# Optimization experiments

Measured on AMD Instinct MI355X. Metric: run time of the kernel, lower is better.

The kernel has to match this reference:

```python
import jax, jax.numpy as jnp
import numpy as np

LN_EPS = 1e-12


def setup_inputs() -> dict:
    key = jax.random.key(0)
    ks = jax.random.split(key, 6)
    B, S, H = 32, 512, 768
    P, K = 76, 64
    V, E = 50257, 768
    return {
        "sequence_data": jax.random.normal(ks[0], (B, S, H), dtype=jnp.float32),
        "masked_positions": jax.random.randint(ks[1], (B, P), 0, S, dtype=jnp.int64),
        "candidate_sets": jax.random.randint(ks[2], (B, P, K), 0, V, dtype=jnp.int64),
        "embedding_table": jax.random.normal(ks[3], (V, E), dtype=jnp.float32) * 0.02,
        "dense_w": jax.random.normal(ks[4], (H, E), dtype=jnp.float32) * (1.0 / np.sqrt(H)),
        "dense_b": jnp.zeros((E,), dtype=jnp.float32),
        "ln_gamma": jnp.ones((E,), dtype=jnp.float32),
        "ln_beta": jnp.zeros((E,), dtype=jnp.float32),
    }


def reference(sequence_data, masked_positions, candidate_sets, embedding_table,
              dense_w, dense_b, ln_gamma, ln_beta):
    # Gather masked positions: [B, P, H]
    gathered = jnp.take_along_axis(
        sequence_data, masked_positions[:, :, None], axis=1)
    # Dense (no activation), then LayerNorm (eps=1e-12)
    lm = jnp.einsum('bph,he->bpe', gathered, dense_w) + dense_b
    mu = jnp.mean(lm, axis=-1, keepdims=True)
    var = jnp.mean(jnp.square(lm - mu), axis=-1, keepdims=True)
    lm = (lm - mu) * jax.lax.rsqrt(var + LN_EPS) * ln_gamma + ln_beta
    # Candidate embedding gather: [B, P, K, E]
    cand = embedding_table[candidate_sets]
    # Inner products -> logits [B, P, K]
    logits = jnp.einsum('bpe,bpke->bpk', lm, cand)
    return logits
```

## Files before the change

kernel.cpp:

```cpp
#include <hip/hip_runtime.h>

typedef __attribute__((ext_vector_type(8))) short bf16x8;
typedef __attribute__((ext_vector_type(4))) float f32x4;

#define HH 768
#define EE 768
#define BB 32
#define SS 512
#define PP 76
#define KCAND 64
#define MM (BB * PP)
#define VV 50257
#define NC (MM * KCAND)
#define CAP 16
#define OVF_CAP 4096

#define OFF_WT    0u
#define OFF_AG    1179648u
#define OFF_LM    4915200u
#define OFF_LMN   12386304u
#define OFF_CUR   16121856u
#define OFF_PERM2 16322896u
#define OFF_OVF   19539344u

#define WT_BLOCKS 576
#define AG_BLOCKS 304
#define ZR_BLOCKS 197
#define GEMM_BLOCKS 456
#define SC_BLOCKS 608
#define ROW_BLOCKS 12565
#define OVF_BLOCKS 32

__device__ inline unsigned short f2bf(float f) {
    unsigned int u = __float_as_uint(f);
    u += 0x7fffu + ((u >> 16) & 1u);
    return (unsigned short)(u >> 16);
}
__device__ inline float bf2f(unsigned short h) {
    return __uint_as_float(((unsigned int)h) << 16);
}

__global__ __launch_bounds__(256) void prep_kernel(
    const float* __restrict__ W, unsigned short* __restrict__ Wt,
    const float* __restrict__ seq, const int* __restrict__ mpos,
    unsigned short* __restrict__ Ag, int* __restrict__ cursor) {
    const int bid = blockIdx.x;
    if (bid < WT_BLOCKS) {
        __shared__ float tile[32][33];
        const int h0 = (bid % 24) * 32, e0 = (bid / 24) * 32;
        const int c = threadIdx.x & 31, r = threadIdx.x >> 5;
#pragma unroll
        for (int rr = r; rr < 32; rr += 8)
            tile[rr][c] = W[(size_t)(h0 + rr) * EE + e0 + c];
        __syncthreads();
#pragma unroll
        for (int rr = r; rr < 32; rr += 8)
            Wt[(size_t)(e0 + rr) * HH + h0 + c] = f2bf(tile[c][rr]);
    } else if (bid < WT_BLOCKS + AG_BLOCKS) {
        const int m0 = (bid - WT_BLOCKS) * 8;
        const int t = threadIdx.x;
#pragma unroll
        for (int rr = 0; rr < 8; ++rr) {
            const int m = m0 + rr;
            const int b = m / PP, p = m - b * PP;
            const int ps = mpos[b * PP + p];
            const float* srow = seq + (size_t)(b * SS + ps) * HH;
            unsigned short* drow = Ag + (size_t)m * HH;
#pragma unroll
            for (int j = 0; j < 3; ++j)
                drow[t + j * 256] = f2bf(srow[t + j * 256]);
        }
    } else {
        const int i = (bid - WT_BLOCKS - AG_BLOCKS) * 256 + threadIdx.x;
        if (i <= VV) cursor[i] = 0;
    }
}

__global__ __launch_bounds__(256) void gemm_scatter_kernel(
    const unsigned short* __restrict__ Ag, const unsigned short* __restrict__ Wt,
    float* __restrict__ lm, const int* __restrict__ cand,
    int* __restrict__ cursor, int* __restrict__ perm2, int* __restrict__ ovf) {
    const int bid = blockIdx.x;
    if (bid < GEMM_BLOCKS) {
        __shared__ unsigned short Alds[64][72];
        __shared__ unsigned short Blds[64][72];
        const int bn = bid % 12, bm = bid / 12;
        const int tid = threadIdx.x;
        const int sr = tid >> 2, sc = (tid & 3) * 16;
        const unsigned short* abase = Ag + (size_t)(bm * 64) * HH;
        const unsigned short* bbase = Wt + (size_t)(bn * 64) * HH;
        const int lane = tid & 63, wv = tid >> 6;
        const int wm = wv >> 1, wn = wv & 1;
        const int fr = lane & 15, fq = (lane >> 4) * 8;
        f32x4 acc[2][2] = {};
        for (int kk = 0; kk < HH; kk += 64) {
            __syncthreads();
            *(int4*)&Alds[sr][sc]     = *(const int4*)(abase + (size_t)sr * HH + kk + sc);
            *(int4*)&Alds[sr][sc + 8] = *(const int4*)(abase + (size_t)sr * HH + kk + sc + 8);
            *(int4*)&Blds[sr][sc]     = *(const int4*)(bbase + (size_t)sr * HH + kk + sc);
            *(int4*)&Blds[sr][sc + 8] = *(const int4*)(bbase + (size_t)sr * HH + kk + sc + 8);
            __syncthreads();
#pragma unroll
            for (int ks = 0; ks < 64; ks += 32) {
                bf16x8 af[2], bfr[2];
#pragma unroll
                for (int t = 0; t < 2; ++t)
                    af[t] = *(const bf16x8*)&Alds[wm * 32 + t * 16 + fr][ks + fq];
#pragma unroll
                for (int t = 0; t < 2; ++t)
                    bfr[t] = *(const bf16x8*)&Blds[wn * 32 + t * 16 + fr][ks + fq];
#pragma unroll
                for (int tm = 0; tm < 2; ++tm)
#pragma unroll
                    for (int tn = 0; tn < 2; ++tn)
                        acc[tm][tn] = __builtin_amdgcn_mfma_f32_16x16x32_bf16(
                            af[tm], bfr[tn], acc[tm][tn], 0, 0, 0);
            }
        }
#pragma unroll
        for (int tm = 0; tm < 2; ++tm)
#pragma unroll
            for (int tn = 0; tn < 2; ++tn) {
                const int col = bn * 64 + wn * 32 + tn * 16 + (lane & 15);
                const int rbase = bm * 64 + wm * 32 + tm * 16 + (lane >> 4) * 4;
#pragma unroll
                for (int g = 0; g < 4; ++g)
                    lm[(size_t)(rbase + g) * EE + col] = acc[tm][tn][g];
            }
    } else {
        const int i = (bid - GEMM_BLOCKS) * 256 + threadIdx.x;
        const int row = cand[i];
        const int slot = atomicAdd(&cursor[row], 1);
        if (slot < CAP) {
            perm2[row * CAP + slot] = i;
        } else {
            const int j = atomicAdd(&cursor[VV], 1);
            if (j < OVF_CAP) ovf[j] = i;
        }
    }
}

__global__ __launch_bounds__(256) void ln_kernel(
    const float* __restrict__ lm, const float* __restrict__ bias,
    const float* __restrict__ gamma, const float* __restrict__ beta,
    unsigned short* __restrict__ lmn) {
    const int lane = threadIdx.x & 63;
    const int m = blockIdx.x * 4 + (threadIdx.x >> 6);
    const float4* x4 = (const float4*)(lm + (size_t)m * EE);
    const float4* b4 = (const float4*)bias;
    const float4* g4 = (const float4*)gamma;
    const float4* e4 = (const float4*)beta;
    float x[12], g[12], e[12];
    {
        const float4 X0 = x4[lane * 2], X1 = x4[lane * 2 + 1], X2 = x4[128 + lane];
        const float4 B0 = b4[lane * 2], B1 = b4[lane * 2 + 1], B2 = b4[128 + lane];
        const float4 G0 = g4[lane * 2], G1 = g4[lane * 2 + 1], G2 = g4[128 + lane];
        const float4 E0 = e4[lane * 2], E1 = e4[lane * 2 + 1], E2 = e4[128 + lane];
        x[0]=X0.x+B0.x; x[1]=X0.y+B0.y; x[2]=X0.z+B0.z; x[3]=X0.w+B0.w;
        x[4]=X1.x+B1.x; x[5]=X1.y+B1.y; x[6]=X1.z+B1.z; x[7]=X1.w+B1.w;
        x[8]=X2.x+B2.x; x[9]=X2.y+B2.y; x[10]=X2.z+B2.z; x[11]=X2.w+B2.w;
        g[0]=G0.x; g[1]=G0.y; g[2]=G0.z; g[3]=G0.w;
        g[4]=G1.x; g[5]=G1.y; g[6]=G1.z; g[7]=G1.w;
        g[8]=G2.x; g[9]=G2.y; g[10]=G2.z; g[11]=G2.w;
        e[0]=E0.x; e[1]=E0.y; e[2]=E0.z; e[3]=E0.w;
        e[4]=E1.x; e[5]=E1.y; e[6]=E1.z; e[7]=E1.w;
        e[8]=E2.x; e[9]=E2.y; e[10]=E2.z; e[11]=E2.w;
    }
    float s = 0.f, q = 0.f;
#pragma unroll
    for (int i = 0; i < 12; ++i) { s += x[i]; q += x[i] * x[i]; }
#pragma unroll
    for (int m2 = 32; m2; m2 >>= 1) { s += __shfl_xor(s, m2); q += __shfl_xor(q, m2); }
    const float mu = s * (1.0f / 768.0f);
    const float rstd = rsqrtf(q * (1.0f / 768.0f) - mu * mu + 1e-12f);
    unsigned short o8[8];
#pragma unroll
    for (int i = 0; i < 8; ++i) o8[i] = f2bf((x[i] - mu) * rstd * g[i] + e[i]);
    *(int4*)(lmn + (size_t)m * EE + lane * 8) = *(const int4*)o8;
    unsigned short o4[4];
#pragma unroll
    for (int i = 0; i < 4; ++i) o4[i] = f2bf((x[8 + i] - mu) * rstd * g[8 + i] + e[8 + i]);
    *(ushort2*)(lmn + (size_t)m * EE + 512 + lane * 4) = *(const ushort2*)o4;
    *(ushort2*)(lmn + (size_t)m * EE + 512 + lane * 4 + 2) = *(const ushort2*)(o4 + 2);
}

__global__ __launch_bounds__(256) void group_logits_kernel(
    const float* __restrict__ emb, const unsigned short* __restrict__ lmn,
    const int* __restrict__ cursor, const int* __restrict__ perm2,
    const int* __restrict__ ovf, const int* __restrict__ cand,
    float* __restrict__ out) {
    const int lane = threadIdx.x & 63;
    const int bid = blockIdx.x;
    if (bid < ROW_BLOCKS) {
        const int r = bid * 4 + (threadIdx.x >> 6);
        if (r >= VV) return;
        int c = cursor[r];
        if (c == 0) return;
        if (c > CAP) c = CAP;
        const float4* e4 = (const float4*)(emb + (size_t)r * EE);
        const float4 E0 = e4[lane * 2], E1 = e4[lane * 2 + 1], E2 = e4[128 + lane];
        const int l8 = lane * 8, l4 = 512 + lane * 4;
        const int base = r * CAP;
        for (int o = 0; o < c; o += 4) {
            const int nn = c - o;
            int idxv[4]; bf16x8 c8[4]; ushort4 c4v[4];
#pragma unroll
            for (int j = 0; j < 4; ++j) {
                const int jj = (j < nn) ? j : 0;
                const int idx = perm2[base + o + jj];
                idxv[j] = idx;
                const unsigned short* lrow = lmn + (size_t)(idx >> 6) * EE;
                c8[j] = *(const bf16x8*)(lrow + l8);
                c4v[j] = *(const ushort4*)(lrow + l4);
            }
            float d[4];
#pragma unroll
            for (int j = 0; j < 4; ++j) {
                d[j] = bf2f((unsigned short)c8[j][0]) * E0.x
                     + bf2f((unsigned short)c8[j][1]) * E0.y
                     + bf2f((unsigned short)c8[j][2]) * E0.z
                     + bf2f((unsigned short)c8[j][3]) * E0.w
                     + bf2f((unsigned short)c8[j][4]) * E1.x
                     + bf2f((unsigned short)c8[j][5]) * E1.y
                     + bf2f((unsigned short)c8[j][6]) * E1.z
                     + bf2f((unsigned short)c8[j][7]) * E1.w
                     + bf2f(c4v[j].x) * E2.x + bf2f(c4v[j].y) * E2.y
                     + bf2f(c4v[j].z) * E2.z + bf2f(c4v[j].w) * E2.w;
            }
#pragma unroll
            for (int m2 = 32; m2; m2 >>= 1) {
#pragma unroll
                for (int j = 0; j < 4; ++j) d[j] += __shfl_xor(d[j], m2);
            }
            if (lane == 0) {
#pragma unroll
                for (int j = 0; j < 4; ++j)
                    if (j < nn) out[idxv[j]] = d[j];
            }
        }
    } else {
        const int nov0 = cursor[VV];
        const int nov = nov0 < OVF_CAP ? nov0 : OVF_CAP;
        const int wid = (bid - ROW_BLOCKS) * 4 + (threadIdx.x >> 6);
        const int l8 = lane * 8, l4 = 512 + lane * 4;
        for (int j = wid; j < nov; j += OVF_BLOCKS * 4) {
            const int idx = ovf[j];
            const int r = cand[idx];
            const float4* e4 = (const float4*)(emb + (size_t)r * EE);
            const float4 E0 = e4[lane * 2], E1 = e4[lane * 2 + 1], E2 = e4[128 + lane];
            const unsigned short* lrow = lmn + (size_t)(idx >> 6) * EE;
            const bf16x8 c8 = *(const bf16x8*)(lrow + l8);
            const ushort4 c4v = *(const ushort4*)(lrow + l4);
            float d = bf2f((unsigned short)c8[0]) * E0.x + bf2f((unsigned short)c8[1]) * E0.y
                    + bf2f((unsigned short)c8[2]) * E0.z + bf2f((unsigned short)c8[3]) * E0.w
                    + bf2f((unsigned short)c8[4]) * E1.x + bf2f((unsigned short)c8[5]) * E1.y
                    + bf2f((unsigned short)c8[6]) * E1.z + bf2f((unsigned short)c8[7]) * E1.w
                    + bf2f(c4v.x) * E2.x + bf2f(c4v.y) * E2.y
                    + bf2f(c4v.z) * E2.z + bf2f(c4v.w) * E2.w;
#pragma unroll
            for (int m2 = 32; m2; m2 >>= 1) d += __shfl_xor(d, m2);
            if (lane == 0) out[idx] = d;
        }
    }
}

extern "C" void kernel_launch(void* const* d_in, const int* in_sizes, int n_in,
                              void* d_out, int out_size, void* d_ws, size_t ws_size,
                              hipStream_t stream) {
    const float* seq   = (const float*)d_in[0];
    const int*   mpos  = (const int*)d_in[1];
    const int*   cand  = (const int*)d_in[2];
    const float* emb   = (const float*)d_in[3];
    const float* W     = (const float*)d_in[4];
    const float* bias  = (const float*)d_in[5];
    const float* gamma = (const float*)d_in[6];
    const float* beta  = (const float*)d_in[7];
    float* out = (float*)d_out;

    char* ws = (char*)d_ws;
    unsigned short* Wt   = (unsigned short*)(ws + OFF_WT);
    unsigned short* Ag   = (unsigned short*)(ws + OFF_AG);
    float*          lm   = (float*)(ws + OFF_LM);
    unsigned short* lmn  = (unsigned short*)(ws + OFF_LMN);
    int*            cur  = (int*)(ws + OFF_CUR);
    int*            perm2= (int*)(ws + OFF_PERM2);
    int*            ovf  = (int*)(ws + OFF_OVF);

    prep_kernel<<<WT_BLOCKS + AG_BLOCKS + ZR_BLOCKS, 256, 0, stream>>>(
        W, Wt, seq, mpos, Ag, cur);
    gemm_scatter_kernel<<<GEMM_BLOCKS + SC_BLOCKS, 256, 0, stream>>>(
        Ag, Wt, lm, cand, cur, perm2, ovf);
    ln_kernel<<<MM / 4, 256, 0, stream>>>(lm, bias, gamma, beta, lmn);
    group_logits_kernel<<<ROW_BLOCKS + OVF_BLOCKS, 256, 0, stream>>>(
        emb, lmn, cur, perm2, ovf, cand, out);
}
```

Measured before the change: 280.1 us.

## Assign 16 lanes per embedding row instead of a full wavefront in logits kernel

The grouped logits kernel now maps each embedding row to a 16-lane group, so one 64-lane wave handles four vocabulary rows instead of one. Each lane keeps 48 embedding floats in registers, loaded with nontemporal hints, and handles two candidates per iteration with a 16-lane shuffle reduction. The goal is to cut idle wave overhead and the launch of many empty-row blocks, since most rows have only about three candidates. The cost is higher register pressure and divergence when rows in the same wave have different candidate counts.

```diff
diff --git a/kernel.cpp b/kernel.cpp
--- a/kernel.cpp
+++ b/kernel.cpp
@@ -28,7 +28,7 @@
 #define ZR_BLOCKS 197
 #define GEMM_BLOCKS 456
 #define SC_BLOCKS 608
-#define ROW_BLOCKS 12565
+#define GROUP_BLOCKS 3142
 #define OVF_BLOCKS 32
 
 __device__ inline unsigned short f2bf(float f) {
@@ -189,64 +189,73 @@
     const int* __restrict__ cursor, const int* __restrict__ perm2,
     const int* __restrict__ ovf, const int* __restrict__ cand,
     float* __restrict__ out) {
-    const int lane = threadIdx.x & 63;
+    const int tid = threadIdx.x;
+    const int lane = tid & 63;
     const int bid = blockIdx.x;
-    if (bid < ROW_BLOCKS) {
-        const int r = bid * 4 + (threadIdx.x >> 6);
-        if (r >= VV) return;
-        int c = cursor[r];
-        if (c == 0) return;
-        if (c > CAP) c = CAP;
-        const float4* e4 = (const float4*)(emb + (size_t)r * EE);
-        const float4 E0 = e4[lane * 2], E1 = e4[lane * 2 + 1], E2 = e4[128 + lane];
-        const int l8 = lane * 8, l4 = 512 + lane * 4;
-        const int base = r * CAP;
-        for (int o = 0; o < c; o += 4) {
-            const int nn = c - o;
-            int idxv[4]; bf16x8 c8[4]; ushort4 c4v[4];
-#pragma unroll
-            for (int j = 0; j < 4; ++j) {
-                const int jj = (j < nn) ? j : 0;
-                const int idx = perm2[base + o + jj];
-                idxv[j] = idx;
-                const unsigned short* lrow = lmn + (size_t)(idx >> 6) * EE;
-                c8[j] = *(const bf16x8*)(lrow + l8);
-                c4v[j] = *(const ushort4*)(lrow + l4);
+    if (bid < GROUP_BLOCKS) {
+        const int l16 = lane & 15;
+        const int r = bid * 16 + (tid >> 4);
+        int c = (r < VV) ? cursor[r] : 0;
+        if (__ballot(c != 0) == 0ULL) return;
+        if (c != 0) {
+            if (c > CAP) c = CAP;
+            const f32x4* e4 = (const f32x4*)(emb + (size_t)r * EE);
+            f32x4 EA[6], EB[6];
+#pragma unroll
+            for (int j = 0; j < 6; ++j) {
+                EA[j] = __builtin_nontemporal_load(e4 + 2 * l16 + 32 * j);
+                EB[j] = __builtin_nontemporal_load(e4 + 2 * l16 + 32 * j + 1);
             }
-            float d[4];
-#pragma unroll
-            for (int j = 0; j < 4; ++j) {
-                d[j] = bf2f((unsigned short)c8[j][0]) * E0.x
-                     + bf2f((unsigned short)c8[j][1]) * E0.y
-                     + bf2f((unsigned short)c8[j][2]) * E0.z
-                     + bf2f((unsigned short)c8[j][3]) * E0.w
-                     + bf2f((unsigned short)c8[j][4]) * E1.x
-                     + bf2f((unsigned short)c8[j][5]) * E1.y
-                     + bf2f((unsigned short)c8[j][6]) * E1.z
-                     + bf2f((unsigned short)c8[j][7]) * E1.w
-                     + bf2f(c4v[j].x) * E2.x + bf2f(c4v[j].y) * E2.y
-                     + bf2f(c4v[j].z) * E2.z + bf2f(c4v[j].w) * E2.w;
-            }
-#pragma unroll
-            for (int m2 = 32; m2; m2 >>= 1) {
-#pragma unroll
-                for (int j = 0; j < 4; ++j) d[j] += __shfl_xor(d[j], m2);
-            }
-            if (lane == 0) {
-#pragma unroll
-                for (int j = 0; j < 4; ++j)
-                    if (j < nn) out[idxv[j]] = d[j];
+            const int base = r * CAP;
+            const int loff = l16 * 8;
+            for (int o = 0; o < c; o += 2) {
+                const int has2 = (c - o) > 1;
+                const int i0 = perm2[base + o];
+                const int i1 = perm2[base + o + (has2 ? 1 : 0)];
+                const unsigned short* r0 = lmn + (size_t)(i0 >> 6) * EE + loff;
+                const unsigned short* r1 = lmn + (size_t)(i1 >> 6) * EE + loff;
+                bf16x8 a0[6], a1[6];
+#pragma unroll
+                for (int j = 0; j < 6; ++j) {
+                    a0[j] = *(const bf16x8*)(r0 + j * 128);
+                    a1[j] = *(const bf16x8*)(r1 + j * 128);
+                }
+                float d0 = 0.f, d1 = 0.f;
+#pragma unroll
+                for (int j = 0; j < 6; ++j) {
+                    const float* ea = (const float*)&EA[j];
+                    const float* eb = (const float*)&EB[j];
+#pragma unroll
+                    for (int t = 0; t < 4; ++t) {
+                        d0 += bf2f((unsigned short)a0[j][t]) * ea[t];
+                        d1 += bf2f((unsigned short)a1[j][t]) * ea[t];
+                    }
+#pragma unroll
+                    for (int t = 0; t < 4; ++t) {
+                        d0 += bf2f((unsigned short)a0[j][4 + t]) * eb[t];
+                        d1 += bf2f((unsigned short)a1[j][4 + t]) * eb[t];
+                    }
+                }
+#pragma unroll
+                for (int m2 = 1; m2 < 16; m2 <<= 1) {
+                    d0 += __shfl_xor(d0, m2);
+                    d1 += __shfl_xor(d1, m2);
+                }
+                if (l16 == 0) {
+                    out[i0] = d0;
+                    if (has2) out[i1] = d1;
+                }
             }
         }
     } else {
         const int nov0 = cursor[VV];
         const int nov = nov0 < OVF_CAP ? nov0 : OVF_CAP;
-        const int wid = (bid - ROW_BLOCKS) * 4 + (threadIdx.x >> 6);
+        const int wid = (bid - GROUP_BLOCKS) * 4 + (threadIdx.x >> 6);
         const int l8 = lane * 8, l4 = 512 + lane * 4;
         for (int j = wid; j < nov; j += OVF_BLOCKS * 4) {
             const int idx = ovf[j];
-            const int r = cand[idx];
-            const float4* e4 = (const float4*)(emb + (size_t)r * EE);
+            const int rr = cand[idx];
+            const float4* e4 = (const float4*)(emb + (size_t)rr * EE);
             const float4 E0 = e4[lane * 2], E1 = e4[lane * 2 + 1], E2 = e4[128 + lane];
             const unsigned short* lrow = lmn + (size_t)(idx >> 6) * EE;
             const bf16x8 c8 = *(const bf16x8*)(lrow + l8);
@@ -291,6 +300,6 @@
     gemm_scatter_kernel<<<GEMM_BLOCKS + SC_BLOCKS, 256, 0, stream>>>(
         Ag, Wt, lm, cand, cur, perm2, ovf);
     ln_kernel<<<MM / 4, 256, 0, stream>>>(lm, bias, gamma, beta, lmn);
-    group_logits_kernel<<<ROW_BLOCKS + OVF_BLOCKS, 256, 0, stream>>>(
+    group_logits_kernel<<<GROUP_BLOCKS + OVF_BLOCKS, 256, 0, stream>>>(
         emb, lmn, cur, perm2, ovf, cand, out);
 }
```

Result: no change. 282.0 us (+0.7%).

## Fuse LayerNorm into per-row candidate logits and drop embedding-row bucketing

Applied to the files above, without the earlier changes.

Removes the atomic bucketing of candidates by embedding row, along with its cursor zeroing and overflow path. The separate LayerNorm kernel is folded into a new per-(b,p) kernel. That kernel normalises the dense output into shared memory as bf16, then directly gathers the 64 candidate embedding rows and computes the dot products with 16-lane groups. This cuts two kernel stages, the atomics and the random re-reads of normalised rows. In exchange, embedding rows that several candidates share are no longer read once each, so more total embedding traffic falls on the caches and HBM.

```diff
diff --git a/kernel.cpp b/kernel.cpp
--- a/kernel.cpp
+++ b/kernel.cpp
@@ -11,25 +11,14 @@
 #define KCAND 64
 #define MM (BB * PP)
 #define VV 50257
-#define NC (MM * KCAND)
-#define CAP 16
-#define OVF_CAP 4096
 
 #define OFF_WT    0u
 #define OFF_AG    1179648u
 #define OFF_LM    4915200u
-#define OFF_LMN   12386304u
-#define OFF_CUR   16121856u
-#define OFF_PERM2 16322896u
-#define OFF_OVF   19539344u
 
 #define WT_BLOCKS 576
 #define AG_BLOCKS 304
-#define ZR_BLOCKS 197
 #define GEMM_BLOCKS 456
-#define SC_BLOCKS 608
-#define ROW_BLOCKS 12565
-#define OVF_BLOCKS 32
 
 __device__ inline unsigned short f2bf(float f) {
     unsigned int u = __float_as_uint(f);
@@ -43,7 +32,7 @@
 __global__ __launch_bounds__(256) void prep_kernel(
     const float* __restrict__ W, unsigned short* __restrict__ Wt,
     const float* __restrict__ seq, const int* __restrict__ mpos,
-    unsigned short* __restrict__ Ag, int* __restrict__ cursor) {
+    unsigned short* __restrict__ Ag) {
     const int bid = blockIdx.x;
     if (bid < WT_BLOCKS) {
         __shared__ float tile[32][33];
@@ -56,7 +45,7 @@
 #pragma unroll
         for (int rr = r; rr < 32; rr += 8)
             Wt[(size_t)(e0 + rr) * HH + h0 + c] = f2bf(tile[c][rr]);
-    } else if (bid < WT_BLOCKS + AG_BLOCKS) {
+    } else {
         const int m0 = (bid - WT_BLOCKS) * 8;
         const int t = threadIdx.x;
 #pragma unroll
@@ -70,196 +59,119 @@
             for (int j = 0; j < 3; ++j)
                 drow[t + j * 256] = f2bf(srow[t + j * 256]);
         }
-    } else {
-        const int i = (bid - WT_BLOCKS - AG_BLOCKS) * 256 + threadIdx.x;
-        if (i <= VV) cursor[i] = 0;
     }
 }
 
-__global__ __launch_bounds__(256) void gemm_scatter_kernel(
+__global__ __launch_bounds__(256) void gemm_kernel(
     const unsigned short* __restrict__ Ag, const unsigned short* __restrict__ Wt,
-    float* __restrict__ lm, const int* __restrict__ cand,
-    int* __restrict__ cursor, int* __restrict__ perm2, int* __restrict__ ovf) {
+    float* __restrict__ lm) {
+    __shared__ unsigned short Alds[64][72];
+    __shared__ unsigned short Blds[64][72];
     const int bid = blockIdx.x;
-    if (bid < GEMM_BLOCKS) {
-        __shared__ unsigned short Alds[64][72];
-        __shared__ unsigned short Blds[64][72];
-        const int bn = bid % 12, bm = bid / 12;
-        const int tid = threadIdx.x;
-        const int sr = tid >> 2, sc = (tid & 3) * 16;
-        const unsigned short* abase = Ag + (size_t)(bm * 64) * HH;
-        const unsigned short* bbase = Wt + (size_t)(bn * 64) * HH;
-        const int lane = tid & 63, wv = tid >> 6;
-        const int wm = wv >> 1, wn = wv & 1;
-        const int fr = lane & 15, fq = (lane >> 4) * 8;
-        f32x4 acc[2][2] = {};
-        for (int kk = 0; kk < HH; kk += 64) {
-            __syncthreads();
-            *(int4*)&Alds[sr][sc]     = *(const int4*)(abase + (size_t)sr * HH + kk + sc);
-            *(int4*)&Alds[sr][sc + 8] = *(const int4*)(abase + (size_t)sr * HH + kk + sc + 8);
-            *(int4*)&Blds[sr][sc]     = *(const int4*)(bbase + (size_t)sr * HH + kk + sc);
-            *(int4*)&Blds[sr][sc + 8] = *(const int4*)(bbase + (size_t)sr * HH + kk + sc + 8);
-            __syncthreads();
-#pragma unroll
-            for (int ks = 0; ks < 64; ks += 32) {
-                bf16x8 af[2], bfr[2];
-#pragma unroll
-                for (int t = 0; t < 2; ++t)
-                    af[t] = *(const bf16x8*)&Alds[wm * 32 + t * 16 + fr][ks + fq];
-#pragma unroll
-                for (int t = 0; t < 2; ++t)
-                    bfr[t] = *(const bf16x8*)&Blds[wn * 32 + t * 16 + fr][ks + fq];
-#pragma unroll
-                for (int tm = 0; tm < 2; ++tm)
-#pragma unroll
-                    for (int tn = 0; tn < 2; ++tn)
-                        acc[tm][tn] = __builtin_amdgcn_mfma_f32_16x16x32_bf16(
-                            af[tm], bfr[tn], acc[tm][tn], 0, 0, 0);
-            }
-        }
-#pragma unroll
-        for (int tm = 0; tm < 2; ++tm)
-#pragma unroll
-            for (int tn = 0; tn < 2; ++tn) {
-                const int col = bn * 64 + wn * 32 + tn * 16 + (lane & 15);
-                const int rbase = bm * 64 + wm * 32 + tm * 16 + (lane >> 4) * 4;
-#pragma unroll
-                for (int g = 0; g < 4; ++g)
-                    lm[(size_t)(rbase + g) * EE + col] = acc[tm][tn][g];
-            }
-    } else {
-        const int i = (bid - GEMM_BLOCKS) * 256 + threadIdx.x;
-        const int row = cand[i];
-        const int slot = atomicAdd(&cursor[row], 1);
-        if (slot < CAP) {
-            perm2[row * CAP + slot] = i;
-        } else {
-            const int j = atomicAdd(&cursor[VV], 1);
-            if (j < OVF_CAP) ovf[j] = i;
+    const int bn = bid % 12, bm = bid / 12;
+    const int tid = threadIdx.x;
+    const int sr = tid >> 2, sc = (tid & 3) * 16;
+    const unsigned short* abase = Ag + (size_t)(bm * 64) * HH;
+    const unsigned short* bbase = Wt + (size_t)(bn * 64) * HH;
+    const int lane = tid & 63, wv = tid >> 6;
+    const int wm = wv >> 1, wn = wv & 1;
+    const int fr = lane & 15, fq = (lane >> 4) * 8;
+    f32x4 acc[2][2] = {};
+    for (int kk = 0; kk < HH; kk += 64) {
+        __syncthreads();
+        *(int4*)&Alds[sr][sc]     = *(const int4*)(abase + (size_t)sr * HH + kk + sc);
+        *(int4*)&Alds[sr][sc + 8] = *(const int4*)(abase + (size_t)sr * HH + kk + sc + 8);
+        *(int4*)&Blds[sr][sc]     = *(const int4*)(bbase + (size_t)sr * HH + kk + sc);
+        *(int4*)&Blds[sr][sc + 8] = *(const int4*)(bbase + (size_t)sr * HH + kk + sc + 8);
+        __syncthreads();
+#pragma unroll
+        for (int ks = 0; ks < 64; ks += 32) {
+            bf16x8 af[2], bfr[2];
+#pragma unroll
+            for (int t = 0; t < 2; ++t)
+                af[t] = *(const bf16x8*)&Alds[wm * 32 + t * 16 + fr][ks + fq];
+#pragma unroll
+            for (int t = 0; t < 2; ++t)
+                bfr[t] = *(const bf16x8*)&Blds[wn * 32 + t * 16 + fr][ks + fq];
+#pragma unroll
+            for (int tm = 0; tm < 2; ++tm)
+#pragma unroll
+                for (int tn = 0; tn < 2; ++tn)
+                    acc[tm][tn] = __builtin_amdgcn_mfma_f32_16x16x32_bf16(
+                        af[tm], bfr[tn], acc[tm][tn], 0, 0, 0);
         }
     }
-}
-
-__global__ __launch_bounds__(256) void ln_kernel(
+#pragma unroll
+    for (int tm = 0; tm < 2; ++tm)
+#pragma unroll
+        for (int tn = 0; tn < 2; ++tn) {
+            const int col = bn * 64 + wn * 32 + tn * 16 + (lane & 15);
+            const int rbase = bm * 64 + wm * 32 + tm * 16 + (lane >> 4) * 4;
+#pragma unroll
+            for (int g = 0; g < 4; ++g)
+                lm[(size_t)(rbase + g) * EE + col] = acc[tm][tn][g];
+        }
+}
+
+__global__ __launch_bounds__(256) void mrow_logits_kernel(
     const float* __restrict__ lm, const float* __restrict__ bias,
     const float* __restrict__ gamma, const float* __restrict__ beta,
-    unsigned short* __restrict__ lmn) {
-    const int lane = threadIdx.x & 63;
-    const int m = blockIdx.x * 4 + (threadIdx.x >> 6);
-    const float4* x4 = (const float4*)(lm + (size_t)m * EE);
-    const float4* b4 = (const float4*)bias;
-    const float4* g4 = (const float4*)gamma;
-    const float4* e4 = (const float4*)beta;
-    float x[12], g[12], e[12];
-    {
-        const float4 X0 = x4[lane * 2], X1 = x4[lane * 2 + 1], X2 = x4[128 + lane];
-        const float4 B0 = b4[lane * 2], B1 = b4[lane * 2 + 1], B2 = b4[128 + lane];
-        const float4 G0 = g4[lane * 2], G1 = g4[lane * 2 + 1], G2 = g4[128 + lane];
-        const float4 E0 = e4[lane * 2], E1 = e4[lane * 2 + 1], E2 = e4[128 + lane];
-        x[0]=X0.x+B0.x; x[1]=X0.y+B0.y; x[2]=X0.z+B0.z; x[3]=X0.w+B0.w;
-        x[4]=X1.x+B1.x; x[5]=X1.y+B1.y; x[6]=X1.z+B1.z; x[7]=X1.w+B1.w;
-        x[8]=X2.x+B2.x; x[9]=X2.y+B2.y; x[10]=X2.z+B2.z; x[11]=X2.w+B2.w;
-        g[0]=G0.x; g[1]=G0.y; g[2]=G0.z; g[3]=G0.w;
-        g[4]=G1.x; g[5]=G1.y; g[6]=G1.z; g[7]=G1.w;
-        g[8]=G2.x; g[9]=G2.y; g[10]=G2.z; g[11]=G2.w;
-        e[0]=E0.x; e[1]=E0.y; e[2]=E0.z; e[3]=E0.w;
-        e[4]=E1.x; e[5]=E1.y; e[6]=E1.z; e[7]=E1.w;
-        e[8]=E2.x; e[9]=E2.y; e[10]=E2.z; e[11]=E2.w;
-    }
-    float s = 0.f, q = 0.f;
-#pragma unroll
-    for (int i = 0; i < 12; ++i) { s += x[i]; q += x[i] * x[i]; }
-#pragma unroll
-    for (int m2 = 32; m2; m2 >>= 1) { s += __shfl_xor(s, m2); q += __shfl_xor(q, m2); }
+    const int* __restrict__ cand, const float* __restrict__ emb,
+    float* __restrict__ out) {
+    const int m = blockIdx.x;
+    const int t = threadIdx.x;
+    __shared__ unsigned short lmn_s[EE];
+    __shared__ float redS[4], redQ[4];
+
+    const float x0 = lm[(size_t)m * EE + t]       + bias[t];
+    const float x1 = lm[(size_t)m * EE + t + 256] + bias[t + 256];
+    const float x2 = lm[(size_t)m * EE + t + 512] + bias[t + 512];
+    float s = x0 + x1 + x2;
+    float q = x0 * x0 + x1 * x1 + x2 * x2;
+#pragma unroll
+    for (int w = 32; w; w >>= 1) { s += __shfl_xor(s, w); q += __shfl_xor(q, w); }
+    const int lane = t & 63, wv = t >> 6;
+    if (lane == 0) { redS[wv] = s; redQ[wv] = q; }
+    __syncthreads();
+    s = redS[0] + redS[1] + redS[2] + redS[3];
+    q = redQ[0] + redQ[1] + redQ[2] + redQ[3];
     const float mu = s * (1.0f / 768.0f);
     const float rstd = rsqrtf(q * (1.0f / 768.0f) - mu * mu + 1e-12f);
-    unsigned short o8[8];
-#pragma unroll
-    for (int i = 0; i < 8; ++i) o8[i] = f2bf((x[i] - mu) * rstd * g[i] + e[i]);
-    *(int4*)(lmn + (size_t)m * EE + lane * 8) = *(const int4*)o8;
-    unsigned short o4[4];
-#pragma unroll
-    for (int i = 0; i < 4; ++i) o4[i] = f2bf((x[8 + i] - mu) * rstd * g[8 + i] + e[8 + i]);
-    *(ushort2*)(lmn + (size_t)m * EE + 512 + lane * 4) = *(const ushort2*)o4;
-    *(ushort2*)(lmn + (size_t)m * EE + 512 + lane * 4 + 2) = *(const ushort2*)(o4 + 2);
-}
-
-__global__ __launch_bounds__(256) void group_logits_kernel(
-    const float* __restrict__ emb, const unsigned short* __restrict__ lmn,
-    const int* __restrict__ cursor, const int* __restrict__ perm2,
-    const int* __restrict__ ovf, const int* __restrict__ cand,
-    float* __restrict__ out) {
-    const int lane = threadIdx.x & 63;
-    const int bid = blockIdx.x;
-    if (bid < ROW_BLOCKS) {
-        const int r = bid * 4 + (threadIdx.x >> 6);
-        if (r >= VV) return;
-        int c = cursor[r];
-        if (c == 0) return;
-        if (c > CAP) c = CAP;
-        const float4* e4 = (const float4*)(emb + (size_t)r * EE);
-        const float4 E0 = e4[lane * 2], E1 = e4[lane * 2 + 1], E2 = e4[128 + lane];
-        const int l8 = lane * 8, l4 = 512 + lane * 4;
-        const int base = r * CAP;
-        for (int o = 0; o < c; o += 4) {
-            const int nn = c - o;
-            int idxv[4]; bf16x8 c8[4]; ushort4 c4v[4];
-#pragma unroll
-            for (int j = 0; j < 4; ++j) {
-                const int jj = (j < nn) ? j : 0;
-                const int idx = perm2[base + o + jj];
-                idxv[j] = idx;
-                const unsigned short* lrow = lmn + (size_t)(idx >> 6) * EE;
-                c8[j] = *(const bf16x8*)(lrow + l8);
-                c4v[j] = *(const ushort4*)(lrow + l4);
-            }
-            float d[4];
-#pragma unroll
-            for (int j = 0; j < 4; ++j) {
-                d[j] = bf2f((unsigned short)c8[j][0]) * E0.x
-                     + bf2f((unsigned short)c8[j][1]) * E0.y
-                     + bf2f((unsigned short)c8[j][2]) * E0.z
-                     + bf2f((unsigned short)c8[j][3]) * E0.w
-                     + bf2f((unsigned short)c8[j][4]) * E1.x
-                     + bf2f((unsigned short)c8[j][5]) * E1.y
-                     + bf2f((unsigned short)c8[j][6]) * E1.z
-                     + bf2f((unsigned short)c8[j][7]) * E1.w
-                     + bf2f(c4v[j].x) * E2.x + bf2f(c4v[j].y) * E2.y
-                     + bf2f(c4v[j].z) * E2.z + bf2f(c4v[j].w) * E2.w;
-            }
-#pragma unroll
-            for (int m2 = 32; m2; m2 >>= 1) {
-#pragma unroll
-                for (int j = 0; j < 4; ++j) d[j] += __shfl_xor(d[j], m2);
-            }
-            if (lane == 0) {
-#pragma unroll
-                for (int j = 0; j < 4; ++j)
-                    if (j < nn) out[idxv[j]] = d[j];
-            }
-        }
-    } else {
-        const int nov0 = cursor[VV];
-        const int nov = nov0 < OVF_CAP ? nov0 : OVF_CAP;
-        const int wid = (bid - ROW_BLOCKS) * 4 + (threadIdx.x >> 6);
-        const int l8 = lane * 8, l4 = 512 + lane * 4;
-        for (int j = wid; j < nov; j += OVF_BLOCKS * 4) {
-            const int idx = ovf[j];
-            const int r = cand[idx];
-            const float4* e4 = (const float4*)(emb + (size_t)r * EE);
-            const float4 E0 = e4[lane * 2], E1 = e4[lane * 2 + 1], E2 = e4[128 + lane];
-            const unsigned short* lrow = lmn + (size_t)(idx >> 6) * EE;
-            const bf16x8 c8 = *(const bf16x8*)(lrow + l8);
-            const ushort4 c4v = *(const ushort4*)(lrow + l4);
-            float d = bf2f((unsigned short)c8[0]) * E0.x + bf2f((unsigned short)c8[1]) * E0.y
-                    + bf2f((unsigned short)c8[2]) * E0.z + bf2f((unsigned short)c8[3]) * E0.w
-                    + bf2f((unsigned short)c8[4]) * E1.x + bf2f((unsigned short)c8[5]) * E1.y
-                    + bf2f((unsigned short)c8[6]) * E1.z + bf2f((unsigned short)c8[7]) * E1.w
-                    + bf2f(c4v.x) * E2.x + bf2f(c4v.y) * E2.y
-                    + bf2f(c4v.z) * E2.z + bf2f(c4v.w) * E2.w;
-#pragma unroll
-            for (int m2 = 32; m2; m2 >>= 1) d += __shfl_xor(d, m2);
-            if (lane == 0) out[idx] = d;
+    lmn_s[t]       = f2bf((x0 - mu) * rstd * gamma[t]       + beta[t]);
+    lmn_s[t + 256] = f2bf((x1 - mu) * rstd * gamma[t + 256] + beta[t + 256]);
+    lmn_s[t + 512] = f2bf((x2 - mu) * rstd * gamma[t + 512] + beta[t + 512]);
+    __syncthreads();
+
+    const int g = t >> 4, l16 = t & 15;
+    ushort4 ln4[12];
+#pragma unroll
+    for (int j = 0; j < 12; ++j)
+        ln4[j] = *(const ushort4*)&lmn_s[4 * l16 + 64 * j];
+
+    const f32x4* e4 = (const f32x4*)emb;
+    const int cb = m * 64 + g;
+#pragma unroll
+    for (int kk = 0; kk < 4; kk += 2) {
+        const int r0 = cand[cb + 16 * kk];
+        const int r1 = cand[cb + 16 * kk + 16];
+        const f32x4* p0 = e4 + (size_t)r0 * 192 + l16;
+        const f32x4* p1 = e4 + (size_t)r1 * 192 + l16;
+        f32x4 A0[12], A1[12];
+#pragma unroll
+        for (int j = 0; j < 12; ++j) { A0[j] = p0[16 * j]; A1[j] = p1[16 * j]; }
+        float d0 = 0.f, d1 = 0.f;
+#pragma unroll
+        for (int j = 0; j < 12; ++j) {
+            d0 += bf2f(ln4[j].x) * A0[j][0] + bf2f(ln4[j].y) * A0[j][1]
+                + bf2f(ln4[j].z) * A0[j][2] + bf2f(ln4[j].w) * A0[j][3];
+            d1 += bf2f(ln4[j].x) * A1[j][0] + bf2f(ln4[j].y) * A1[j][1]
+                + bf2f(ln4[j].z) * A1[j][2] + bf2f(ln4[j].w) * A1[j][3];
+        }
+#pragma unroll
+        for (int w = 1; w < 16; w <<= 1) { d0 += __shfl_xor(d0, w); d1 += __shfl_xor(d1, w); }
+        if (l16 == 0) {
+            out[cb + 16 * kk] = d0;
+            out[cb + 16 * kk + 16] = d1;
         }
     }
 }
@@ -278,19 +190,11 @@
     float* out = (float*)d_out;
 
     char* ws = (char*)d_ws;
-    unsigned short* Wt   = (unsigned short*)(ws + OFF_WT);
-    unsigned short* Ag   = (unsigned short*)(ws + OFF_AG);
-    float*          lm   = (float*)(ws + OFF_LM);
-    unsigned short* lmn  = (unsigned short*)(ws + OFF_LMN);
-    int*            cur  = (int*)(ws + OFF_CUR);
-    int*            perm2= (int*)(ws + OFF_PERM2);
-    int*            ovf  = (int*)(ws + OFF_OVF);
-
-    prep_kernel<<<WT_BLOCKS + AG_BLOCKS + ZR_BLOCKS, 256, 0, stream>>>(
-        W, Wt, seq, mpos, Ag, cur);
-    gemm_scatter_kernel<<<GEMM_BLOCKS + SC_BLOCKS, 256, 0, stream>>>(
-        Ag, Wt, lm, cand, cur, perm2, ovf);
-    ln_kernel<<<MM / 4, 256, 0, stream>>>(lm, bias, gamma, beta, lmn);
-    group_logits_kernel<<<ROW_BLOCKS + OVF_BLOCKS, 256, 0, stream>>>(
-        emb, lmn, cur, perm2, ovf, cand, out);
-}
+    unsigned short* Wt = (unsigned short*)(ws + OFF_WT);
+    unsigned short* Ag = (unsigned short*)(ws + OFF_AG);
+    float*          lm = (float*)(ws + OFF_LM);
+
+    prep_kernel<<<WT_BLOCKS + AG_BLOCKS, 256, 0, stream>>>(W, Wt, seq, mpos, Ag);
+    gemm_kernel<<<GEMM_BLOCKS, 256, 0, stream>>>(Ag, Wt, lm);
+    mrow_logits_kernel<<<MM, 256, 0, stream>>>(lm, bias, gamma, beta, cand, emb, out);
+}
```

Result: slower. 292.3 us (+4.4%).
